# Kernel optimization log

Measured on AMD Instinct MI355X. Metric: run time of the kernel, lower is better.

Reference implementation:

```python
import jax, jax.numpy as jnp
import numpy as np

B, S, DM, H = 2, 2048, 1024, 16        # dim_model = d_model//2 = 1024
WINDOW, DILATION, N_GLOBAL = 513, 2, 32
HD = DM // H
NEG = -1e9


def build_mask(n, window_size, dilation, global_idx):
    # dilated local window: |i-j| <= (window//2)*dilation and (i-j) % dilation == 0
    i = jnp.arange(n)[:, None]
    j = jnp.arange(n)[None, :]
    d = j - i
    half = window_size // 2
    local = (jnp.abs(d) <= half * dilation) & (jnp.mod(d, dilation) == 0)
    g = jnp.zeros((n,), bool).at[global_idx].set(True)
    # symmetric global token mask: global rows and columns fully attend
    return local | g[:, None] | g[None, :]


def setup_inputs() -> dict:
    key = jax.random.key(0)
    ks = jax.random.split(key, 9)
    std = 0.02
    inp = {
        "q": jax.random.normal(ks[0], (B, S, DM), jnp.float32),
        "k": jax.random.normal(ks[1], (B, S, DM), jnp.float32),
        "v": jax.random.normal(ks[2], (B, S, DM), jnp.float32),
        "Wq": jax.random.normal(ks[3], (DM, DM), jnp.float32) * std,
        "Wk": jax.random.normal(ks[4], (DM, DM), jnp.float32) * std,
        "Wv": jax.random.normal(ks[5], (DM, DM), jnp.float32) * std,
        "Wo": jax.random.normal(ks[6], (DM, DM), jnp.float32) * std,
        "bq": jnp.zeros((DM,), jnp.float32),
        "bk": jnp.zeros((DM,), jnp.float32),
        "bv": jnp.zeros((DM,), jnp.float32),
        "bo": jnp.zeros((DM,), jnp.float32),
        "global_idx": jax.random.randint(ks[7], (N_GLOBAL,), 0, S, jnp.int64)
        if jax.config.jax_enable_x64 else jax.random.randint(ks[7], (N_GLOBAL,), 0, S, jnp.int32),
    }
    return inp


def reference(q, k, v, Wq, Wk, Wv, Wo, bq, bk, bv, bo, global_idx):
    def split(x):  # [B,S,DM] -> [B,H,S,HD]
        return x.reshape(B, S, H, HD).transpose(0, 2, 1, 3)

    qh = split(q @ Wq.T + bq)
    kh = split(k @ Wk.T + bk)
    vh = split(v @ Wv.T + bv)

    scores = jnp.einsum("bhqd,bhkd->bhqk", qh, kh) / jnp.sqrt(jnp.asarray(HD, qh.dtype))
    mask = build_mask(S, WINDOW, DILATION, global_idx)  # [S,S] bool
    scores = jnp.where(mask[None, None], scores, NEG)
    attn = jax.nn.softmax(scores, axis=-1)
    out = jnp.einsum("bhqk,bhkd->bhqd", attn, vh)
    out = out.transpose(0, 2, 1, 3).reshape(B, S, DM)
    return out @ Wo.T + bo
```

## Files before the change

### kernel.cpp

```cpp
#include <hip/hip_runtime.h>
#include <hip/hip_bf16.h>
#include <math.h>

#define BB 2
#define SS 2048
#define DMM 1024
#define HH 16
#define HDD 64
#define NGLOB 32
#define MM 4096
#define SCALE2 0.18033688f

typedef __attribute__((ext_vector_type(8))) short short8;
typedef __attribute__((ext_vector_type(4))) float float4v;

__device__ __forceinline__ short f2bf(float f) {
    union { float f; unsigned u; } x; x.f = f;
    unsigned r = (x.u + 0x7fffu + ((x.u >> 16) & 1u)) >> 16;
    return (short)r;
}

#define ASYNC16(gp, lp) __builtin_amdgcn_global_load_lds( \
    (__attribute__((address_space(1))) void*)(gp), \
    (__attribute__((address_space(3))) void*)(lp), 16, 0, 0)

#define VSL(dim, key) ((dim) * 40 + (((((key) >> 3) ^ (((dim) >> 3) & 3)) << 3) | ((key) & 7)))

__global__ __launch_bounds__(256)
void convert_all(const float* __restrict__ q, const float* __restrict__ k,
                 const float* __restrict__ v,
                 const float* __restrict__ w0, const float* __restrict__ w1,
                 const float* __restrict__ w2, const float* __restrict__ w3,
                 short* __restrict__ abf, short* __restrict__ wbf,
                 const int* __restrict__ gidx, int* __restrict__ g,
                 int* __restrict__ glist, int* __restrict__ gcount) {
    int z = blockIdx.y;
    int t = threadIdx.x;
    if (z == 7) {
        if (blockIdx.x != 0) return;
        for (int i = t; i < SS; i += 256) g[i] = 0;
        if (t == 0) *gcount = 0;
        __syncthreads();
        if (t < NGLOB) {
            int j = gidx[t];
            if (j >= 0 && j < SS) g[j] = 1;
        }
        __syncthreads();
        for (int j = t; j < SS; j += 256) {
            if (g[j]) {
                int p = atomicAdd(gcount, 1);
                glist[p] = j;
            }
        }
        return;
    }
    const float* src;
    short* dst;
    size_t n;
    if (z < 3) {
        src = (z == 0) ? q : (z == 1) ? k : v;
        dst = abf + (size_t)z * ((size_t)MM * DMM);
        n = (size_t)MM * DMM;
    } else {
        int y = z - 3;
        src = (y == 0) ? w0 : (y == 1) ? w1 : (y == 2) ? w2 : w3;
        dst = wbf + (size_t)y * ((size_t)DMM * DMM);
        n = (size_t)DMM * DMM;
    }
    size_t i = ((size_t)blockIdx.x * 256 + t) * 8;
    if (i >= n) return;
    float4 a = *(const float4*)(src + i);
    float4 b = *(const float4*)(src + i + 4);
    short8 s;
    s[0]=f2bf(a.x); s[1]=f2bf(a.y); s[2]=f2bf(a.z); s[3]=f2bf(a.w);
    s[4]=f2bf(b.x); s[5]=f2bf(b.y); s[6]=f2bf(b.z); s[7]=f2bf(b.w);
    *(short8*)(dst + i) = s;
}

template<int OBF, int HEADSPLIT>
__global__ __launch_bounds__(512, 2)
void gemm256(const short* __restrict__ Abase, const short* __restrict__ Wbase,
             const float* __restrict__ b0, const float* __restrict__ b1,
             const float* __restrict__ b2,
             void* __restrict__ O0p, void* __restrict__ O1p, void* __restrict__ O2p) {
    __shared__ short As[2][256 * 64];
    __shared__ short Ws[2][256 * 64];

    int t = threadIdx.x;
    int z = blockIdx.y;
    const short* A    = Abase + (size_t)z * ((size_t)MM * DMM);
    const short* W    = Wbase + (size_t)z * ((size_t)DMM * DMM);
    const float* bias = (z == 0) ? b0 : (z == 1) ? b1 : b2;
    void* outp        = (z == 0) ? O0p : (z == 1) ? O1p : O2p;

    int bid = blockIdx.x;
    int mt = bid & 15, nt = bid >> 4;
    int m0 = mt * 256, n0 = nt * 256;

    int lane = t & 63, w = t >> 6;
    int quad = lane >> 4, col = lane & 15;
    int wm = (w >> 2) * 128;
    int wn = (w & 3) * 64;

    float4v acc[8][4];
    #pragma unroll
    for (int i = 0; i < 8; i++)
        #pragma unroll
        for (int j = 0; j < 4; j++) acc[i][j] = (float4v){0, 0, 0, 0};

    int srow = t >> 3;
    int scol = ((t & 7) ^ (srow & 7)) * 8;
    const short* Ap = A + (size_t)(m0 + srow) * DMM + scol;
    const short* Wp = W + (size_t)(n0 + srow) * DMM + scol;

    #define STAGE256(bf, tt) do { size_t kk = (size_t)(tt) * 64; \
        ASYNC16(Ap + kk,                        &As[bf][t * 8]); \
        ASYNC16(Ap +  64 * (size_t)DMM + kk,    &As[bf][4096  + t * 8]); \
        ASYNC16(Ap + 128 * (size_t)DMM + kk,    &As[bf][8192  + t * 8]); \
        ASYNC16(Ap + 192 * (size_t)DMM + kk,    &As[bf][12288 + t * 8]); \
        ASYNC16(Wp + kk,                        &Ws[bf][t * 8]); \
        ASYNC16(Wp +  64 * (size_t)DMM + kk,    &Ws[bf][4096  + t * 8]); \
        ASYNC16(Wp + 128 * (size_t)DMM + kk,    &Ws[bf][8192  + t * 8]); \
        ASYNC16(Wp + 192 * (size_t)DMM + kk,    &Ws[bf][12288 + t * 8]); \
    } while (0)

    int c7 = col & 7;

    STAGE256(0, 0);

    for (int it = 0; it < 16; it++) {
        int cur = it & 1;
        if (it < 15) {
            STAGE256(cur ^ 1, it + 1);
            asm volatile("s_waitcnt vmcnt(8)" ::: "memory");
        } else {
            asm volatile("s_waitcnt vmcnt(0)" ::: "memory");
        }
        __builtin_amdgcn_s_barrier();

        short8 bF[4][2];
        #pragma unroll
        for (int j = 0; j < 4; j++) {
            int rB = (wn + 16 * j + col) * 64;
            #pragma unroll
            for (int ks = 0; ks < 2; ks++)
                bF[j][ks] = *(short8*)&Ws[cur][rB + ((((ks << 2) | quad) ^ c7) << 3)];
        }

        #pragma unroll
        for (int p = 0; p < 4; p++) {
            if (p) __builtin_amdgcn_s_barrier();
            short8 aF[2][2];
            #pragma unroll
            for (int u = 0; u < 2; u++) {
                int rA = (wm + 16 * (2 * p + u) + col) * 64;
                #pragma unroll
                for (int ks = 0; ks < 2; ks++)
                    aF[u][ks] = *(short8*)&As[cur][rA + ((((ks << 2) | quad) ^ c7) << 3)];
            }
            __builtin_amdgcn_s_setprio(1);
            #pragma unroll
            for (int ks = 0; ks < 2; ks++)
                #pragma unroll
                for (int u = 0; u < 2; u++)
                    #pragma unroll
                    for (int j = 0; j < 4; j++)
                        acc[2 * p + u][j] = __builtin_amdgcn_mfma_f32_16x16x32_bf16(
                            aF[u][ks], bF[j][ks], acc[2 * p + u][j], 0, 0, 0);
            __builtin_amdgcn_s_setprio(0);
        }
        __builtin_amdgcn_s_barrier();
    }
    #undef STAGE256

    #pragma unroll
    for (int i = 0; i < 8; i++) {
        #pragma unroll
        for (int j = 0; j < 4; j++) {
            int n = n0 + wn + 16 * j + col;
            float bn = bias[n];
            #pragma unroll
            for (int r = 0; r < 4; r++) {
                int m = m0 + wm + 16 * i + quad * 4 + r;
                float val = acc[i][j][r] + bn;
                size_t idx;
                if (HEADSPLIT) {
                    int b = m >> 11;
                    int s = m & 2047;
                    int h = n >> 6;
                    int hd = n & 63;
                    idx = (((size_t)b * HH + h) * SS + s) * HDD + hd;
                } else {
                    idx = (size_t)m * DMM + n;
                }
                if (OBF) ((short*)outp)[idx] = f2bf(val);
                else     ((float*)outp)[idx] = val;
            }
        }
    }
}

__global__ __launch_bounds__(512, 2)
void gemm128wo(const short* __restrict__ A, const short* __restrict__ W,
               const float* __restrict__ bias, float* __restrict__ out) {
    __shared__ short As[2][128 * 64];
    __shared__ short Ws[2][128 * 64];

    int t = threadIdx.x;
    int bid = blockIdx.x;
    int mt = bid & 31, nt = bid >> 5;
    int m0 = mt * 128, n0 = nt * 128;

    int lane = t & 63, w = t >> 6;
    int quad = lane >> 4, col = lane & 15;
    int wm = (w >> 2) * 64;
    int wn = (w & 3) * 32;

    float4v acc[4][2];
    #pragma unroll
    for (int i = 0; i < 4; i++)
        #pragma unroll
        for (int j = 0; j < 2; j++) acc[i][j] = (float4v){0, 0, 0, 0};

    int srow = t >> 3;
    int scol = ((t & 7) ^ (srow & 7)) * 8;
    const short* Ap = A + (size_t)(m0 + srow) * DMM + scol;
    const short* Wp = W + (size_t)(n0 + srow) * DMM + scol;

    #define STAGEWO(bf, tt) do { size_t kk = (size_t)(tt) * 64; \
        ASYNC16(Ap + kk,                      &As[bf][t * 8]); \
        ASYNC16(Ap + 64 * (size_t)DMM + kk,   &As[bf][4096 + t * 8]); \
        ASYNC16(Wp + kk,                      &Ws[bf][t * 8]); \
        ASYNC16(Wp + 64 * (size_t)DMM + kk,   &Ws[bf][4096 + t * 8]); \
    } while (0)

    int c7 = col & 7;

    STAGEWO(0, 0);

    for (int it = 0; it < 16; it++) {
        int cur = it & 1;
        if (it < 15) {
            STAGEWO(cur ^ 1, it + 1);
            asm volatile("s_waitcnt vmcnt(4)" ::: "memory");
        } else {
            asm volatile("s_waitcnt vmcnt(0)" ::: "memory");
        }
        __builtin_amdgcn_s_barrier();

        short8 bF[2][2];
        #pragma unroll
        for (int j = 0; j < 2; j++) {
            int rB = (wn + 16 * j + col) * 64;
            #pragma unroll
            for (int ks = 0; ks < 2; ks++)
                bF[j][ks] = *(short8*)&Ws[cur][rB + ((((ks << 2) | quad) ^ c7) << 3)];
        }

        #pragma unroll
        for (int p = 0; p < 2; p++) {
            if (p) __builtin_amdgcn_s_barrier();
            short8 aF[2][2];
            #pragma unroll
            for (int u = 0; u < 2; u++) {
                int rA = (wm + 16 * (2 * p + u) + col) * 64;
                #pragma unroll
                for (int ks = 0; ks < 2; ks++)
                    aF[u][ks] = *(short8*)&As[cur][rA + ((((ks << 2) | quad) ^ c7) << 3)];
            }
            __builtin_amdgcn_s_setprio(1);
            #pragma unroll
            for (int ks = 0; ks < 2; ks++)
                #pragma unroll
                for (int u = 0; u < 2; u++)
                    #pragma unroll
                    for (int j = 0; j < 2; j++)
                        acc[2 * p + u][j] = __builtin_amdgcn_mfma_f32_16x16x32_bf16(
                            aF[u][ks], bF[j][ks], acc[2 * p + u][j], 0, 0, 0);
            __builtin_amdgcn_s_setprio(0);
        }
        __builtin_amdgcn_s_barrier();
    }
    #undef STAGEWO

    #pragma unroll
    for (int i = 0; i < 4; i++) {
        #pragma unroll
        for (int j = 0; j < 2; j++) {
            int n = n0 + wn + 16 * j + col;
            float bn = bias[n];
            #pragma unroll
            for (int r = 0; r < 4; r++) {
                int m = m0 + wm + 16 * i + quad * 4 + r;
                out[(size_t)m * DMM + n] = acc[i][j][r] + bn;
            }
        }
    }
}

__global__ __launch_bounds__(256)
void attn_fused(const short* __restrict__ qh, const short* __restrict__ kh,
                const short* __restrict__ vh, const int* __restrict__ glist,
                const int* __restrict__ gcount, short* __restrict__ ao,
                float* __restrict__ pl, float* __restrict__ pO) {
    __shared__ __align__(16) char smem[29184];
    int t = threadIdx.x;
    int bid = blockIdx.x;
    int nG = *gcount;

    if (bid < 1024) {
        short* Qs = (short*)smem;
        short* Ks = Qs + 64 * 72;
        short* Vt = Ks + 32 * 72;
        short* Ps = Vt + 64 * 40;
        int*   gjs = (int*)(Ps + 4 * 16 * 40);

        int xcd = bid & 7, idx = bid >> 3;
        int gl  = idx >> 4;
        int qt  = idx & 15;
        int gid = xcd * 8 + gl;
        int z   = gid >> 4;
        int h   = gid & 15;
        int b = z >> 1, p = z & 1;
        int qq0 = qt * 64;

        const short* Qb = qh + ((size_t)(b * HH + h) * SS) * HDD;
        const short* Kb = kh + ((size_t)(b * HH + h) * SS) * HDD;
        const short* Vb = vh + ((size_t)(b * HH + h) * SS) * HDD;

        int row8 = t >> 3;
        int dim8 = (t & 7) * 8;

        #pragma unroll
        for (int rr = 0; rr < 2; rr++) {
            int row = rr * 32 + row8;
            int i = 2 * (qq0 + row) + p;
            short8 qv = *(const short8*)(Qb + (size_t)i * HDD + dim8);
            *(short8*)&Qs[row * 72 + dim8] = qv;
        }
        if (t < 32) gjs[t] = (t < nG) ? glist[t] : -1000000;
        __syncthreads();

        int lane = t & 63, w = t >> 6;
        int quad = lane >> 4, col = lane & 15;

        short8 qf0 = *(short8*)&Qs[(16 * w + col) * 72 + quad * 8];
        short8 qf1 = *(short8*)&Qs[(16 * w + col) * 72 + 32 + quad * 8];

        float4v O0 = {0,0,0,0}, O1 = {0,0,0,0}, O2 = {0,0,0,0}, O3 = {0,0,0,0};
        float lst[4] = {0.f, 0.f, 0.f, 0.f};

        short8 kvP, vvP, kvN, vvN;
        {
            int srow = 2 * (qq0 - 256 + row8) + p;
            srow = srow < 0 ? 0 : (srow > SS - 1 ? SS - 1 : srow);
            kvP = *(const short8*)(Kb + (size_t)srow * HDD + dim8);
            vvP = *(const short8*)(Vb + (size_t)srow * HDD + dim8);
        }

        for (int c = 0; c < 19; c++) {
            __syncthreads();
            *(short8*)&Ks[row8 * 72 + dim8] = kvP;
            #pragma unroll
            for (int j = 0; j < 8; j++) {
                int d = dim8 + j;
                Vt[VSL(d, row8)] = vvP[j];
            }
            if (c < 18) {
                int cn = c + 1;
                int ch0n = qq0 - 256 + cn * 32;
                int srow;
                if (cn < 18) srow = 2 * (ch0n + row8) + p;
                else         srow = (row8 < nG) ? gjs[row8] : 0;
                srow = srow < 0 ? 0 : (srow > SS - 1 ? SS - 1 : srow);
                kvN = *(const short8*)(Kb + (size_t)srow * HDD + dim8);
                vvN = *(const short8*)(Vb + (size_t)srow * HDD + dim8);
            }
            __syncthreads();

            int ch0 = qq0 - 256 + c * 32;

            short8 kA0 = *(short8*)&Ks[col * 72 + quad * 8];
            short8 kA1 = *(short8*)&Ks[col * 72 + 32 + quad * 8];
            short8 kB0 = *(short8*)&Ks[(16 + col) * 72 + quad * 8];
            short8 kB1 = *(short8*)&Ks[(16 + col) * 72 + 32 + quad * 8];
            float4v sA = {0,0,0,0}, sB = {0,0,0,0};
            sA = __builtin_amdgcn_mfma_f32_16x16x32_bf16(qf0, kA0, sA, 0, 0, 0);
            sA = __builtin_amdgcn_mfma_f32_16x16x32_bf16(qf1, kA1, sA, 0, 0, 0);
            sB = __builtin_amdgcn_mfma_f32_16x16x32_bf16(qf0, kB0, sB, 0, 0, 0);
            sB = __builtin_amdgcn_mfma_f32_16x16x32_bf16(qf1, kB1, sB, 0, 0, 0);

            if (c < 18) {
                int nlo = -ch0;
                int nhi = 1023 - ch0;
                #pragma unroll
                for (int r = 0; r < 4; r++) {
                    int qq = qq0 + 16 * w + quad * 4 + r;
                    int u  = qq - ch0;
                    int lo = max(u - 256, nlo);
                    int hi = min(u + 256, nhi);
                    bool vA = (col >= lo) && (col <= hi);
                    bool vB = (col + 16 >= lo) && (col + 16 <= hi);
                    float pa = vA ? exp2f(sA[r] * SCALE2) : 0.f;
                    float pb = vB ? exp2f(sB[r] * SCALE2) : 0.f;
                    lst[r] += pa + pb;
                    Ps[(w * 16 + quad * 4 + r) * 40 + col]      = f2bf(pa);
                    Ps[(w * 16 + quad * 4 + r) * 40 + col + 16] = f2bf(pb);
                }
            } else {
                #pragma unroll
                for (int r = 0; r < 4; r++) {
                    int qq = qq0 + 16 * w + quad * 4 + r;
                    int i = 2 * qq + p;
                    int jA = gjs[col], jB = gjs[col + 16];
                    int dA = jA - i, dB = jB - i;
                    int aA = dA < 0 ? -dA : dA;
                    int aB = dB < 0 ? -dB : dB;
                    bool vA = (jA >= 0) && !((aA <= 512) && ((dA & 1) == 0));
                    bool vB = (jB >= 0) && !((aB <= 512) && ((dB & 1) == 0));
                    float pa = vA ? exp2f(sA[r] * SCALE2) : 0.f;
                    float pb = vB ? exp2f(sB[r] * SCALE2) : 0.f;
                    lst[r] += pa + pb;
                    Ps[(w * 16 + quad * 4 + r) * 40 + col]      = f2bf(pa);
                    Ps[(w * 16 + quad * 4 + r) * 40 + col + 16] = f2bf(pb);
                }
            }
            asm volatile("s_waitcnt lgkmcnt(0)" ::: "memory");

            short8 pf  = *(short8*)&Ps[(w * 16 + col) * 40 + quad * 8];
            short8 vf0 = *(short8*)&Vt[(col) * 40 + ((quad ^ ((col >> 3) & 3)) << 3)];
            short8 vf1 = *(short8*)&Vt[(16 + col) * 40 + ((quad ^ (((16 + col) >> 3) & 3)) << 3)];
            short8 vf2 = *(short8*)&Vt[(32 + col) * 40 + ((quad ^ (((32 + col) >> 3) & 3)) << 3)];
            short8 vf3 = *(short8*)&Vt[(48 + col) * 40 + ((quad ^ (((48 + col) >> 3) & 3)) << 3)];
            O0 = __builtin_amdgcn_mfma_f32_16x16x32_bf16(pf, vf0, O0, 0, 0, 0);
            O1 = __builtin_amdgcn_mfma_f32_16x16x32_bf16(pf, vf1, O1, 0, 0, 0);
            O2 = __builtin_amdgcn_mfma_f32_16x16x32_bf16(pf, vf2, O2, 0, 0, 0);
            O3 = __builtin_amdgcn_mfma_f32_16x16x32_bf16(pf, vf3, O3, 0, 0, 0);

            kvP = kvN; vvP = vvN;
        }

        #pragma unroll
        for (int r = 0; r < 4; r++) {
            float l = lst[r];
            #pragma unroll
            for (int mk = 1; mk < 16; mk <<= 1) l += __shfl_xor(l, mk);
            float inv = 1.0f / l;
            int q = 16 * w + quad * 4 + r;
            int i = 2 * (qq0 + q) + p;
            short* dst = ao + ((size_t)b * SS + i) * DMM + h * HDD;
            dst[col]      = f2bf(O0[r] * inv);
            dst[col + 16] = f2bf(O1[r] * inv);
            dst[col + 32] = f2bf(O2[r] * inv);
            dst[col + 48] = f2bf(O3[r] * inv);
        }
    } else {
        short* Qs  = (short*)smem;
        short* Ksf = Qs + 32 * 72;
        short* Vtf = Ksf + 2 * 32 * 72;
        short* Ps  = Vtf + 2 * 64 * 40;

        int r0 = bid - 1024;
        int s = r0 & 7, h = (r0 >> 3) & 15, b = r0 >> 7;

        const short* Qb = qh + ((size_t)(b * HH + h) * SS) * HDD;
        const short* Kb = kh + ((size_t)(b * HH + h) * SS) * HDD;
        const short* Vb = vh + ((size_t)(b * HH + h) * SS) * HDD;

        int row8 = t >> 3, dim8 = (t & 7) * 8;
        {
            int cq = row8 < nG ? row8 : 0;
            int src = glist[cq];
            short8 qv = *(const short8*)(Qb + (size_t)src * HDD + dim8);
            *(short8*)&Qs[row8 * 72 + dim8] = qv;
        }
        __syncthreads();

        int lane = t & 63, w = t >> 6;
        int quad = lane >> 4, col = lane & 15;
        int g = w >> 1, qt = w & 1;

        short8 qf0 = *(short8*)&Qs[(qt * 16 + col) * 72 + quad * 8];
        short8 qf1 = *(short8*)&Qs[(qt * 16 + col) * 72 + 32 + quad * 8];

        float4v O0 = {0,0,0,0}, O1 = {0,0,0,0}, O2 = {0,0,0,0}, O3 = {0,0,0,0};
        float lst[4] = {0.f, 0.f, 0.f, 0.f};

        int js0 = s * 256;
        for (int it = 0; it < 4; it++) {
            __syncthreads();
            int r64 = t >> 2, dimb = (t & 3) * 16;
            int j = js0 + it * 64 + r64;
            const short* kp = Kb + (size_t)j * HDD + dimb;
            const short* vp = Vb + (size_t)j * HDD + dimb;
            short8 k0 = *(const short8*)kp, k1 = *(const short8*)(kp + 8);
            short8 v0 = *(const short8*)vp, v1 = *(const short8*)(vp + 8);
            int half = r64 >> 5, r32 = r64 & 31;
            short* Ksh = Ksf + half * (32 * 72);
            short* Vth = Vtf + half * (64 * 40);
            *(short8*)&Ksh[r32 * 72 + dimb]     = k0;
            *(short8*)&Ksh[r32 * 72 + dimb + 8] = k1;
            #pragma unroll
            for (int u = 0; u < 8; u++) {
                int d = dimb + u;
                Vth[VSL(d, r32)] = v0[u];
            }
            #pragma unroll
            for (int u = 0; u < 8; u++) {
                int d = dimb + 8 + u;
                Vth[VSL(d, r32)] = v1[u];
            }
            __syncthreads();

            short* Ksg = Ksf + g * (32 * 72);
            short* Vtg = Vtf + g * (64 * 40);
            short8 kA0 = *(short8*)&Ksg[col * 72 + quad * 8];
            short8 kA1 = *(short8*)&Ksg[col * 72 + 32 + quad * 8];
            short8 kB0 = *(short8*)&Ksg[(16 + col) * 72 + quad * 8];
            short8 kB1 = *(short8*)&Ksg[(16 + col) * 72 + 32 + quad * 8];
            float4v sA = {0,0,0,0}, sB = {0,0,0,0};
            sA = __builtin_amdgcn_mfma_f32_16x16x32_bf16(qf0, kA0, sA, 0, 0, 0);
            sA = __builtin_amdgcn_mfma_f32_16x16x32_bf16(qf1, kA1, sA, 0, 0, 0);
            sB = __builtin_amdgcn_mfma_f32_16x16x32_bf16(qf0, kB0, sB, 0, 0, 0);
            sB = __builtin_amdgcn_mfma_f32_16x16x32_bf16(qf1, kB1, sB, 0, 0, 0);

            #pragma unroll
            for (int r = 0; r < 4; r++) {
                float pa = exp2f(sA[r] * SCALE2);
                float pb = exp2f(sB[r] * SCALE2);
                lst[r] += pa + pb;
                Ps[(w * 16 + quad * 4 + r) * 40 + col]      = f2bf(pa);
                Ps[(w * 16 + quad * 4 + r) * 40 + col + 16] = f2bf(pb);
            }
            asm volatile("s_waitcnt lgkmcnt(0)" ::: "memory");

            short8 pf  = *(short8*)&Ps[(w * 16 + col) * 40 + quad * 8];
            short8 vf0 = *(short8*)&Vtg[(col) * 40 + ((quad ^ ((col >> 3) & 3)) << 3)];
            short8 vf1 = *(short8*)&Vtg[(16 + col) * 40 + ((quad ^ (((16 + col) >> 3) & 3)) << 3)];
            short8 vf2 = *(short8*)&Vtg[(32 + col) * 40 + ((quad ^ (((32 + col) >> 3) & 3)) << 3)];
            short8 vf3 = *(short8*)&Vtg[(48 + col) * 40 + ((quad ^ (((48 + col) >> 3) & 3)) << 3)];
            O0 = __builtin_amdgcn_mfma_f32_16x16x32_bf16(pf, vf0, O0, 0, 0, 0);
            O1 = __builtin_amdgcn_mfma_f32_16x16x32_bf16(pf, vf1, O1, 0, 0, 0);
            O2 = __builtin_amdgcn_mfma_f32_16x16x32_bf16(pf, vf2, O2, 0, 0, 0);
            O3 = __builtin_amdgcn_mfma_f32_16x16x32_bf16(pf, vf3, O3, 0, 0, 0);
        }

        int sp = s * 2 + g;
        size_t base = ((size_t)(b * HH + h) * 16 + sp) * 32;
        #pragma unroll
        for (int r = 0; r < 4; r++) {
            float l = lst[r];
            #pragma unroll
            for (int mk = 1; mk < 16; mk <<= 1) l += __shfl_xor(l, mk);
            int q = qt * 16 + quad * 4 + r;
            if (col == 0) pl[base + q] = l;
            float* Od = pO + (base + q) * 64;
            Od[col]      = O0[r];
            Od[col + 16] = O1[r];
            Od[col + 32] = O2[r];
            Od[col + 48] = O3[r];
        }
    }
}

__global__ __launch_bounds__(256)
void global_merge(const float* __restrict__ pl, const float* __restrict__ pO,
                  const int* __restrict__ glist, const int* __restrict__ gcount,
                  short* __restrict__ ao) {
    int h = blockIdx.x, b = blockIdx.y;
    int t = threadIdx.x;
    int d = t & 63, qg = t >> 6;
    int nG = *gcount;
    size_t bh = ((size_t)(b * HH + h) * 16) * 32;

    for (int q = qg; q < nG; q += 4) {
        float L = 0.f, acc = 0.f;
        #pragma unroll
        for (int sp = 0; sp < 16; sp++) {
            L   += pl[bh + sp * 32 + q];
            acc += pO[(bh + sp * 32 + q) * 64 + d];
        }
        int i = glist[q];
        ao[((size_t)b * SS + i) * DMM + h * HDD + d] = f2bf(acc / L);
    }
}

extern "C" void kernel_launch(void* const* d_in, const int* in_sizes, int n_in,
                              void* d_out, int out_size, void* d_ws, size_t ws_size,
                              hipStream_t stream) {
    const float* q  = (const float*)d_in[0];
    const float* k  = (const float*)d_in[1];
    const float* v  = (const float*)d_in[2];
    const float* Wq = (const float*)d_in[3];
    const float* Wk = (const float*)d_in[4];
    const float* Wv = (const float*)d_in[5];
    const float* Wo = (const float*)d_in[6];
    const float* bq = (const float*)d_in[7];
    const float* bk = (const float*)d_in[8];
    const float* bv = (const float*)d_in[9];
    const float* bo = (const float*)d_in[10];
    const int* gidx = (const int*)d_in[11];
    float* out = (float*)d_out;

    const size_t NE = (size_t)BB * SS * DMM;
    const size_t WE = (size_t)DMM * DMM;
    int*   g      = (int*)d_ws;
    int*   glist  = g + SS;
    int*   gcount = glist + SS;
    short* qh     = (short*)((char*)d_ws + 32768);
    short* kh     = qh + NE;
    short* vh     = kh + NE;
    short* ao     = vh + NE;
    short* wbf    = ao + NE;
    short* wo     = wbf + 3 * WE;
    short* abf    = wbf + 4 * WE;
    float* pl     = (float*)abf;
    float* pO     = pl + 16384;

    dim3 gc(2048, 8);
    convert_all<<<gc, 256, 0, stream>>>(q, k, v, Wq, Wk, Wv, Wo, abf, wbf,
                                        gidx, g, glist, gcount);

    dim3 gq(64, 3);
    gemm256<1, 1><<<gq, 512, 0, stream>>>(abf, wbf, bq, bk, bv, qh, kh, vh);

    attn_fused<<<1280, 256, 0, stream>>>(qh, kh, vh, glist, gcount, ao, pl, pO);

    dim3 gm(HH, BB);
    global_merge<<<gm, 256, 0, stream>>>(pl, pO, glist, gcount, ao);

    gemm128wo<<<256, 512, 0, stream>>>(ao, wo, bo, out);
}
```

Baseline: 215.6 us.

## Interleave next-tile async loads across MFMA phases in projection GEMM

Replaces the single bulk prefetch of the next K tile with staggered async global-to-LDS loads spread across the four MFMA sub-phases. Partial vmcnt waits let part of the tile become usable earlier, and the end-of-iteration barrier is removed. The aim is to overlap memory traffic with MFMA work more evenly and cut stall time at the start of each iteration. The cost is more barriers per iteration and tricky vmcnt accounting that could race on LDS buffer reuse if the wait counts are wrong.

```diff
diff --git a/kernel.cpp b/kernel.cpp
--- a/kernel.cpp
+++ b/kernel.cpp
@@ -113,30 +113,21 @@
     const short* Ap = A + (size_t)(m0 + srow) * DMM + scol;
     const short* Wp = W + (size_t)(n0 + srow) * DMM + scol;
 
-    #define STAGE256(bf, tt) do { size_t kk = (size_t)(tt) * 64; \
-        ASYNC16(Ap + kk,                        &As[bf][t * 8]); \
-        ASYNC16(Ap +  64 * (size_t)DMM + kk,    &As[bf][4096  + t * 8]); \
-        ASYNC16(Ap + 128 * (size_t)DMM + kk,    &As[bf][8192  + t * 8]); \
-        ASYNC16(Ap + 192 * (size_t)DMM + kk,    &As[bf][12288 + t * 8]); \
-        ASYNC16(Wp + kk,                        &Ws[bf][t * 8]); \
-        ASYNC16(Wp +  64 * (size_t)DMM + kk,    &Ws[bf][4096  + t * 8]); \
-        ASYNC16(Wp + 128 * (size_t)DMM + kk,    &Ws[bf][8192  + t * 8]); \
-        ASYNC16(Wp + 192 * (size_t)DMM + kk,    &Ws[bf][12288 + t * 8]); \
-    } while (0)
+    #define ST_W(bf, tt, h) ASYNC16(Wp + (size_t)(h) * 64 * DMM + (size_t)(tt) * 64, \
+                                    &Ws[bf][(h) * 4096 + t * 8])
+    #define ST_A(bf, tt, h) ASYNC16(Ap + (size_t)(h) * 64 * DMM + (size_t)(tt) * 64, \
+                                    &As[bf][(h) * 4096 + t * 8])
 
     int c7 = col & 7;
 
-    STAGE256(0, 0);
+    ST_W(0, 0, 0); ST_W(0, 0, 1); ST_W(0, 0, 2); ST_W(0, 0, 3);
+    ST_A(0, 0, 0); ST_A(0, 0, 2); ST_A(0, 0, 1); ST_A(0, 0, 3);
+    asm volatile("s_waitcnt vmcnt(2)" ::: "memory");
+    __builtin_amdgcn_s_barrier();
 
     for (int it = 0; it < 16; it++) {
-        int cur = it & 1;
-        if (it < 15) {
-            STAGE256(cur ^ 1, it + 1);
-            asm volatile("s_waitcnt vmcnt(8)" ::: "memory");
-        } else {
-            asm volatile("s_waitcnt vmcnt(0)" ::: "memory");
-        }
-        __builtin_amdgcn_s_barrier();
+        int cur = it & 1, nb = cur ^ 1;
+        bool pf = (it < 15);
 
         short8 bF[4][2];
         #pragma unroll
@@ -149,7 +140,6 @@
 
         #pragma unroll
         for (int p = 0; p < 4; p++) {
-            if (p) __builtin_amdgcn_s_barrier();
             short8 aF[2][2];
             #pragma unroll
             for (int u = 0; u < 2; u++) {
@@ -158,6 +148,13 @@
                 for (int ks = 0; ks < 2; ks++)
                     aF[u][ks] = *(short8*)&As[cur][rA + ((((ks << 2) | quad) ^ c7) << 3)];
             }
+            if (pf) {
+                if (p == 0)      { ST_W(nb, it + 1, 0); ST_W(nb, it + 1, 1); }
+                else if (p == 1) { ST_W(nb, it + 1, 2); ST_W(nb, it + 1, 3); }
+                else if (p == 2) { ST_A(nb, it + 1, 0); ST_A(nb, it + 1, 2); }
+                else             { ST_A(nb, it + 1, 1); ST_A(nb, it + 1, 3); }
+            }
+            __builtin_amdgcn_s_barrier();
             __builtin_amdgcn_s_setprio(1);
             #pragma unroll
             for (int ks = 0; ks < 2; ks++)
@@ -168,10 +165,17 @@
                         acc[2 * p + u][j] = __builtin_amdgcn_mfma_f32_16x16x32_bf16(
                             aF[u][ks], bF[j][ks], acc[2 * p + u][j], 0, 0, 0);
             __builtin_amdgcn_s_setprio(0);
-        }
-        __builtin_amdgcn_s_barrier();
-    }
-    #undef STAGE256
+            if (p == 1) {
+                if (pf) asm volatile("s_waitcnt vmcnt(4)" ::: "memory");
+                else    asm volatile("s_waitcnt vmcnt(0)" ::: "memory");
+            }
+            if (p == 3 && pf)
+                asm volatile("s_waitcnt vmcnt(2)" ::: "memory");
+            __builtin_amdgcn_s_barrier();
+        }
+    }
+    #undef ST_W
+    #undef ST_A
 
     #pragma unroll
     for (int i = 0; i < 8; i++) {
```

Result: faster. 208.4 us (-3.3%).
